# Kernel tuning notes

Hardware: AMD Instinct MI355X
Metric: run time of the kernel (lower is better)

The kernel has to match this reference:

```python
import jax, jax.numpy as jnp
import numpy as np

B, C, D, Q = 256, 1000, 128, 262144
PROTO_M = 0.99   # args.proto_m
TEMP = 0.01      # hardcoded temperature in forward


def setup_inputs() -> dict:
    key = jax.random.key(0)
    ks = jax.random.split(key, 8)
    return {
        'q': jax.random.normal(ks[0], (B, D), jnp.float32),
        'k': jax.random.normal(ks[1], (B, D), jnp.float32),
        'output': jax.random.normal(ks[2], (B, C), jnp.float32),
        'output2': jax.random.normal(ks[3], (B, C), jnp.float32),
        'partial_Y': (jax.random.uniform(ks[4], (B, C)) < 0.1).astype(jnp.float32),
        'prototypes': jax.random.normal(ks[5], (C, D), jnp.float32),
        'queue': jax.random.normal(ks[6], (Q, D), jnp.float32),
        'queue_pseudo': jax.random.uniform(ks[7], (Q,), dtype=jnp.float32),
    }


def reference(q, k, output, output2, partial_Y, prototypes, queue, queue_pseudo):
    # pseudo-label selection: softmax over (detached logits * candidate mask) / T
    predicted_scores = jax.nn.softmax(jax.lax.stop_gradient(output) * partial_Y / TEMP, axis=1)
    pseudo_labels_b = jnp.argmax(predicted_scores, axis=1)  # [B] int

    # prototype scores use prototypes BEFORE the EMA update (mm snapshots values)
    logits_prot = jnp.matmul(jax.lax.stop_gradient(q), prototypes.T)  # [B, C]
    score_prot = jax.nn.softmax(logits_prot, axis=1)

    # sequential per-sample EMA scatter into prototypes (order-dependent on dup labels)
    q_detached = jax.lax.stop_gradient(q)

    def ema_step(protos, xs):
        feat, lab = xs
        new_row = protos[lab] * PROTO_M + (1.0 - PROTO_M) * feat
        return protos.at[lab].set(new_row), None

    protos, _ = jax.lax.scan(ema_step, prototypes, (q_detached, pseudo_labels_b))
    # F.normalize(p=2, dim=1) with eps=1e-12 clamp
    protos = protos / jnp.maximum(jnp.linalg.norm(protos, axis=1, keepdims=True), 1e-12)

    features = jnp.concatenate([q, k, queue], axis=0)  # [2B+Q, D]
    pseudo_labels = jnp.concatenate([
        pseudo_labels_b.astype(jnp.float32),
        pseudo_labels_b.astype(jnp.float32),
        queue_pseudo,
    ], axis=0)  # [2B+Q]

    return (output, output2, features, pseudo_labels, score_prot, protos)
```

## Files before the change

kernel.cpp:

```cpp
#include <hip/hip_runtime.h>
#include <math.h>

#define B 256
#define C 1000
#define D 128
#define QN 262144

#define OFF_FEAT   512000
#define OFF_LBL    34131968
#define OFF_SCORE  34394624
#define OFF_PROTO  34650624

#define N_Q4   (QN * D / 4)
#define N_O4   (B * C / 4)
#define N_F4   (B * D / 4)
#define N_P4   (QN / 4)

#define DST_Q4   ((OFF_FEAT + 2 * B * D) / 4)
#define DST_O24  (B * C / 4)
#define DST_QF4  (OFF_FEAT / 4)
#define DST_KF4  (OFF_FEAT / 4 + N_F4)
#define DST_P4   ((OFF_LBL + 2 * B) / 4)

#define SM_O2  (N_O4)
#define SM_Q   (2 * N_O4)
#define SM_K   (2 * N_O4 + N_F4)
#define SM_P   (2 * N_O4 + 2 * N_F4)
#define SM_TOT (2 * N_O4 + 2 * N_F4 + N_P4)

#define Q_TILES   (N_Q4 / 1024)
#define K1_TILES  640
#define K2_TILES  (Q_TILES - K1_TILES)

#define R_EMA    500
#define R_SCORE  (R_EMA + B)
#define SM_BLKS  ((SM_TOT + 255) / 256)
#define R_SMALL  (R_SCORE + SM_BLKS)
#define K2_GRID  (R_SMALL + K2_TILES)

__global__ __launch_bounds__(256) void k1_kernel(
    const float* __restrict__ output,
    const float* __restrict__ partial_Y,
    const float4* __restrict__ queue,
    int* __restrict__ labels,
    float* __restrict__ out)
{
    const int tid = threadIdx.x;

    if (blockIdx.x >= B) {
        const size_t base = (size_t)(blockIdx.x - B) * 1024 + tid;
        float4* __restrict__ dst = (float4*)out + DST_Q4;
        float4 a = queue[base];
        float4 b = queue[base + 256];
        float4 c = queue[base + 512];
        float4 d = queue[base + 768];
        dst[base]       = a;
        dst[base + 256] = b;
        dst[base + 512] = c;
        dst[base + 768] = d;
        return;
    }

    const int b = blockIdx.x;
    const float* row = output + (size_t)b * C;
    const float* msk = partial_Y + (size_t)b * C;

    float best = -INFINITY;
    int bidx = C;
    for (int c = tid; c < C; c += 256) {
        float v = row[c] * msk[c];
        if (v > best) { best = v; bidx = c; }
    }

    __shared__ float sv[256];
    __shared__ int   si[256];
    sv[tid] = best; si[tid] = bidx;
    __syncthreads();
    for (int s = 128; s > 0; s >>= 1) {
        if (tid < s) {
            float v2 = sv[tid + s]; int i2 = si[tid + s];
            if (v2 > sv[tid] || (v2 == sv[tid] && i2 < si[tid])) {
                sv[tid] = v2; si[tid] = i2;
            }
        }
        __syncthreads();
    }
    if (tid == 0) {
        int lab = si[0];
        labels[b] = lab;
        float f = (float)lab;
        out[OFF_LBL + b]     = f;
        out[OFF_LBL + B + b] = f;
    }
}

__global__ __launch_bounds__(256) void k2_kernel(
    const float* __restrict__ q,
    const float* __restrict__ kk,
    const float* __restrict__ output,
    const float* __restrict__ output2,
    const float* __restrict__ prototypes,
    const float4* __restrict__ queue,
    const float* __restrict__ queue_pseudo,
    const int* __restrict__ labels,
    float* __restrict__ out)
{
    const int bid = blockIdx.x;
    const int tid = threadIdx.x;

    if (bid < R_EMA) {
        __shared__ int   lab[B];
        __shared__ float ss[256];
        const int c = 2 * bid + (tid >> 7);
        const int d = tid & 127;
        for (int i = tid; i < B; i += 256) lab[i] = labels[i];
        __syncthreads();

        float val = prototypes[(size_t)c * D + d];
        for (int b = 0; b < B; ++b) {
            if (lab[b] == c) {
                val = val * 0.99f + 0.01f * q[(size_t)b * D + d];
            }
        }

        ss[tid] = val * val;
        __syncthreads();
        for (int s = 64; s > 0; s >>= 1) {
            if (d < s) ss[tid] += ss[tid + s];
            __syncthreads();
        }
        float r = fmaxf(sqrtf(ss[tid & 128]), 1e-12f);
        out[OFF_PROTO + (size_t)c * D + d] = val / r;
        return;
    }

    if (bid < R_SCORE) {
        const int b = bid - R_EMA;
        __shared__ float qs[D];
        __shared__ float logits[C];
        __shared__ float red[256];
        if (tid < D) qs[tid] = q[(size_t)b * D + tid];
        __syncthreads();

        for (int c = tid; c < C; c += 256) {
            const float4* p4 = (const float4*)(prototypes + (size_t)c * D);
            const float4* q4 = (const float4*)qs;
            float acc = 0.f;
            #pragma unroll
            for (int d = 0; d < D / 4; ++d) {
                float4 pv = p4[d];
                float4 qv = q4[d];
                acc += pv.x * qv.x + pv.y * qv.y + pv.z * qv.z + pv.w * qv.w;
            }
            logits[c] = acc;
        }
        __syncthreads();

        float lm = -INFINITY;
        for (int c = tid; c < C; c += 256) lm = fmaxf(lm, logits[c]);
        red[tid] = lm;
        __syncthreads();
        for (int s = 128; s > 0; s >>= 1) {
            if (tid < s) red[tid] = fmaxf(red[tid], red[tid + s]);
            __syncthreads();
        }
        const float m = red[0];
        __syncthreads();

        float psum = 0.f;
        for (int c = tid; c < C; c += 256) {
            float e = expf(logits[c] - m);
            logits[c] = e;
            psum += e;
        }
        red[tid] = psum;
        __syncthreads();
        for (int s = 128; s > 0; s >>= 1) {
            if (tid < s) red[tid] += red[tid + s];
            __syncthreads();
        }
        const float denom = red[0];

        for (int c = tid; c < C; c += 256)
            out[OFF_SCORE + (size_t)b * C + c] = logits[c] / denom;
        return;
    }

    if (bid < R_SMALL) {
        const size_t i = (size_t)(bid - R_SCORE) * 256 + tid;
        float4* __restrict__ out4 = (float4*)out;
        if (i < SM_O2)       out4[i]                     = ((const float4*)output)[i];
        else if (i < SM_Q)   out4[DST_O24 + (i - SM_O2)] = ((const float4*)output2)[i - SM_O2];
        else if (i < SM_K)   out4[DST_QF4 + (i - SM_Q)]  = ((const float4*)q)[i - SM_Q];
        else if (i < SM_P)   out4[DST_KF4 + (i - SM_K)]  = ((const float4*)kk)[i - SM_K];
        else if (i < SM_TOT) out4[DST_P4 + (i - SM_P)]   = ((const float4*)queue_pseudo)[i - SM_P];
        return;
    }

    const size_t base = ((size_t)(bid - R_SMALL) + K1_TILES) * 1024 + tid;
    float4* __restrict__ dst = (float4*)out + DST_Q4;
    float4 a = queue[base];
    float4 b = queue[base + 256];
    float4 c = queue[base + 512];
    float4 d = queue[base + 768];
    dst[base]       = a;
    dst[base + 256] = b;
    dst[base + 512] = c;
    dst[base + 768] = d;
}

extern "C" void kernel_launch(void* const* d_in, const int* in_sizes, int n_in,
                              void* d_out, int out_size, void* d_ws, size_t ws_size,
                              hipStream_t stream) {
    const float* q            = (const float*)d_in[0];
    const float* k            = (const float*)d_in[1];
    const float* output       = (const float*)d_in[2];
    const float* output2      = (const float*)d_in[3];
    const float* partial_Y    = (const float*)d_in[4];
    const float* prototypes   = (const float*)d_in[5];
    const float* queue        = (const float*)d_in[6];
    const float* queue_pseudo = (const float*)d_in[7];

    float* out  = (float*)d_out;
    int* labels = (int*)d_ws;

    k1_kernel<<<B + K1_TILES, 256, 0, stream>>>(
        output, partial_Y, (const float4*)queue, labels, out);

    k2_kernel<<<K2_GRID, 256, 0, stream>>>(
        q, k, output, output2, prototypes,
        (const float4*)queue, queue_pseudo, labels, out);
}
```

Before: 271.7 us.

## Use persistent work-stealing blocks for queue copy with nontemporal stores

Replaces the per-tile copy blocks in the second kernel with a fixed grid of 2048 persistent blocks. After finishing its compute role (scores, EMA or small copies), each block grabs 8-tile chunks of the queue copy through an atomic counter kept in the workspace. All queue copies now use nontemporal stores to avoid polluting the cache, and the EMA blocks handle four prototype rows each. This is meant to balance the compute roles against the bandwidth-bound copy and cut block launch overhead. It adds atomic contention and relies on the first kernel zeroing the counter.

```diff
diff --git a/kernel.cpp b/kernel.cpp
--- a/kernel.cpp
+++ b/kernel.cpp
@@ -30,13 +30,20 @@
 
 #define Q_TILES   (N_Q4 / 1024)
 #define K1_TILES  640
-#define K2_TILES  (Q_TILES - K1_TILES)
-
-#define R_EMA    500
-#define R_SCORE  (R_EMA + B)
-#define SM_BLKS  ((SM_TOT + 255) / 256)
-#define R_SMALL  (R_SCORE + SM_BLKS)
-#define K2_GRID  (R_SMALL + K2_TILES)
+#define POOL_TILES (Q_TILES - K1_TILES)
+#define CHUNK_T   8
+#define NCHUNK    (POOL_TILES / CHUNK_T)
+
+#define R_SP_END  256
+#define R_EMA_END (R_SP_END + 250)
+#define SM_BLKS   ((SM_TOT + 255) / 256)
+#define R_SM_END  (R_EMA_END + SM_BLKS)
+#define K2_GRID   2048
+
+typedef float f4nt __attribute__((ext_vector_type(4)));
+__device__ __forceinline__ void nt_store(float4* p, float4 v) {
+    __builtin_nontemporal_store(*(const f4nt*)&v, (f4nt*)p);
+}
 
 __global__ __launch_bounds__(256) void k1_kernel(
     const float* __restrict__ output,
@@ -54,12 +61,14 @@
         float4 b = queue[base + 256];
         float4 c = queue[base + 512];
         float4 d = queue[base + 768];
-        dst[base]       = a;
-        dst[base + 256] = b;
-        dst[base + 512] = c;
-        dst[base + 768] = d;
+        nt_store(&dst[base],       a);
+        nt_store(&dst[base + 256], b);
+        nt_store(&dst[base + 512], c);
+        nt_store(&dst[base + 768], d);
         return;
     }
+
+    if (blockIdx.x == 0 && tid == 0) labels[B] = 0;
 
     const int b = blockIdx.x;
     const float* row = output + (size_t)b * C;
@@ -102,43 +111,21 @@
     const float* __restrict__ prototypes,
     const float4* __restrict__ queue,
     const float* __restrict__ queue_pseudo,
-    const int* __restrict__ labels,
+    int* __restrict__ ws,
     float* __restrict__ out)
 {
     const int bid = blockIdx.x;
     const int tid = threadIdx.x;
 
-    if (bid < R_EMA) {
-        __shared__ int   lab[B];
-        __shared__ float ss[256];
-        const int c = 2 * bid + (tid >> 7);
-        const int d = tid & 127;
-        for (int i = tid; i < B; i += 256) lab[i] = labels[i];
-        __syncthreads();
-
-        float val = prototypes[(size_t)c * D + d];
-        for (int b = 0; b < B; ++b) {
-            if (lab[b] == c) {
-                val = val * 0.99f + 0.01f * q[(size_t)b * D + d];
-            }
-        }
-
-        ss[tid] = val * val;
-        __syncthreads();
-        for (int s = 64; s > 0; s >>= 1) {
-            if (d < s) ss[tid] += ss[tid + s];
-            __syncthreads();
-        }
-        float r = fmaxf(sqrtf(ss[tid & 128]), 1e-12f);
-        out[OFF_PROTO + (size_t)c * D + d] = val / r;
-        return;
-    }
-
-    if (bid < R_SCORE) {
-        const int b = bid - R_EMA;
-        __shared__ float qs[D];
-        __shared__ float logits[C];
-        __shared__ float red[256];
+    __shared__ float logits[C];
+    __shared__ float red[256];
+    __shared__ float qs[D];
+    __shared__ int   lab[B];
+    __shared__ float ss[256];
+    __shared__ int   chunk_s;
+
+    if (bid < R_SP_END) {
+        const int b = bid;
         if (tid < D) qs[tid] = q[(size_t)b * D + tid];
         __syncthreads();
 
@@ -183,30 +170,66 @@
 
         for (int c = tid; c < C; c += 256)
             out[OFF_SCORE + (size_t)b * C + c] = logits[c] / denom;
-        return;
-    }
-
-    if (bid < R_SMALL) {
-        const size_t i = (size_t)(bid - R_SCORE) * 256 + tid;
+    }
+    else if (bid < R_EMA_END) {
+        const int ebid = bid - R_SP_END;
+        const int half = tid >> 7;
+        const int d    = tid & 127;
+        for (int i = tid; i < B; i += 256) lab[i] = ws[i];
+        __syncthreads();
+
+        #pragma unroll
+        for (int kcl = 0; kcl < 2; ++kcl) {
+            const int c = 4 * ebid + 2 * kcl + half;
+            float val = prototypes[(size_t)c * D + d];
+            #pragma unroll 8
+            for (int b = 0; b < B; ++b) {
+                if (lab[b] == c) {
+                    val = val * 0.99f + 0.01f * q[(size_t)b * D + d];
+                }
+            }
+            ss[tid] = val * val;
+            __syncthreads();
+            for (int s = 64; s > 0; s >>= 1) {
+                if (d < s) ss[tid] += ss[tid + s];
+                __syncthreads();
+            }
+            float r = fmaxf(sqrtf(ss[half * 128]), 1e-12f);
+            out[OFF_PROTO + (size_t)c * D + d] = val / r;
+            __syncthreads();
+        }
+    }
+    else if (bid < R_SM_END) {
+        const size_t i = (size_t)(bid - R_EMA_END) * 256 + tid;
         float4* __restrict__ out4 = (float4*)out;
         if (i < SM_O2)       out4[i]                     = ((const float4*)output)[i];
         else if (i < SM_Q)   out4[DST_O24 + (i - SM_O2)] = ((const float4*)output2)[i - SM_O2];
         else if (i < SM_K)   out4[DST_QF4 + (i - SM_Q)]  = ((const float4*)q)[i - SM_Q];
         else if (i < SM_P)   out4[DST_KF4 + (i - SM_K)]  = ((const float4*)kk)[i - SM_K];
         else if (i < SM_TOT) out4[DST_P4 + (i - SM_P)]   = ((const float4*)queue_pseudo)[i - SM_P];
-        return;
-    }
-
-    const size_t base = ((size_t)(bid - R_SMALL) + K1_TILES) * 1024 + tid;
+    }
+
     float4* __restrict__ dst = (float4*)out + DST_Q4;
-    float4 a = queue[base];
-    float4 b = queue[base + 256];
-    float4 c = queue[base + 512];
-    float4 d = queue[base + 768];
-    dst[base]       = a;
-    dst[base + 256] = b;
-    dst[base + 512] = c;
-    dst[base + 768] = d;
+    int* cnt = ws + B;
+    for (;;) {
+        __syncthreads();
+        if (tid == 0) chunk_s = atomicAdd(cnt, 1);
+        __syncthreads();
+        const int ch = chunk_s;
+        if (ch >= NCHUNK) break;
+
+        const size_t base = (size_t)(K1_TILES + CHUNK_T * ch) * 1024 + tid;
+        #pragma unroll
+        for (int g = 0; g < 4; ++g) {
+            float4 v[8];
+            #pragma unroll
+            for (int j = 0; j < 8; ++j)
+                v[j] = queue[base + (size_t)(g * 8 + j) * 256];
+            #pragma unroll
+            for (int j = 0; j < 8; ++j)
+                nt_store(&dst[base + (size_t)(g * 8 + j) * 256], v[j]);
+        }
+    }
 }
 
 extern "C" void kernel_launch(void* const* d_in, const int* in_sizes, int n_in,
@@ -221,13 +244,13 @@
     const float* queue        = (const float*)d_in[6];
     const float* queue_pseudo = (const float*)d_in[7];
 
-    float* out  = (float*)d_out;
-    int* labels = (int*)d_ws;
+    float* out = (float*)d_out;
+    int* ws    = (int*)d_ws;
 
     k1_kernel<<<B + K1_TILES, 256, 0, stream>>>(
-        output, partial_Y, (const float4*)queue, labels, out);
+        output, partial_Y, (const float4*)queue, ws, out);
 
     k2_kernel<<<K2_GRID, 256, 0, stream>>>(
         q, k, output, output2, prototypes,
-        (const float4*)queue, queue_pseudo, labels, out);
-}
+        (const float4*)queue, queue_pseudo, ws, out);
+}
```

Result: no change. 273.5 us (+0.6%).
